# Kernel optimization log

Hardware: AMD Instinct MI355X
Metric: run time of the kernel (lower is better)

The kernel has to match this reference:

```python
import jax, jax.numpy as jnp
import numpy as np

B, D, C = 256, 128, 8000
MARGIN = 0.5
SCALE = 64.0
EPS = 1e-12  # tf.nn.l2_normalize epsilon


def _l2_normalize(x, axis):
    # Matches tf.nn.l2_normalize: x * rsqrt(max(sum(x^2), eps))
    sq = jnp.sum(x * x, axis=axis, keepdims=True)
    return x * jax.lax.rsqrt(jnp.maximum(sq, EPS))


def setup_inputs() -> dict:
    key = jax.random.key(0)
    k1, k2, k3 = jax.random.split(key, 3)
    embds = jax.random.normal(k1, (B, D), dtype=jnp.float32)
    w = jax.random.normal(k2, (D, C), dtype=jnp.float32)
    labels = jax.random.randint(k3, (B,), 0, C, dtype=jnp.int32)
    return {"embds": embds, "w": w, "labels": labels}


def reference(embds, w, labels):
    normed_embds = _l2_normalize(embds, axis=1)          # [B, D]
    normed_w = _l2_normalize(w, axis=0)                  # [D, C]
    gr_w = normed_w.T[labels]                            # gather per-label columns -> [B, D]
    # dw[b, d, c] = gr_w[b, d] - normed_w[d, c]
    dw = gr_w[:, :, None] - normed_w[None, :, :]         # [B, D, C]
    normed_dw = _l2_normalize(dw, axis=1)                # normalize over feature dim D
    win = jnp.einsum('bd,bdc->bc', normed_embds, normed_dw)
    penalties = MARGIN - jnp.minimum(MARGIN, win)        # [B, C]
    cos_t = normed_embds @ normed_w                      # [B, C]
    logits = jax.nn.softmax(SCALE * cos_t, axis=-1)
    return (logits, penalties)
```

## Files before the change

kernel.cpp:

```cpp
#include <hip/hip_runtime.h>
#include <math.h>

#define BB 256
#define DD 128
#define CC 8000
#define EPSF 1e-12f
#define SCALEF 64.0f
#define MARGINF 0.5f

__global__ __launch_bounds__(256) void prep1_kernel(
    const float* __restrict__ embds, const float* __restrict__ w,
    float* __restrict__ neT, float* __restrict__ rcol) {
  __shared__ float part[4];
  int bid = blockIdx.x;
  int tid = threadIdx.x;
  if (bid < 128) {
    int half = tid >> 7;
    int d = tid & 127;
    int r = 2 * bid + half;
    float v = embds[r * DD + d];
    float s = v * v;
    #pragma unroll
    for (int off = 32; off; off >>= 1) s += __shfl_down(s, off, 64);
    int wid = tid >> 6;
    if ((tid & 63) == 0) part[wid] = s;
    __syncthreads();
    float total = (half == 0) ? (part[0] + part[1]) : (part[2] + part[3]);
    float rn = rsqrtf(fmaxf(total, EPSF));
    neT[d * BB + r] = v * rn;
  } else {
    int c = (bid - 128) * 256 + tid;
    if (c < CC) {
      float s = 0.f;
      #pragma unroll 4
      for (int d = 0; d < DD; ++d) {
        float v = w[d * CC + c];
        s = fmaf(v, v, s);
      }
      rcol[c] = rsqrtf(fmaxf(s, EPSF));
    }
  }
}

__global__ __launch_bounds__(128) void prep2_kernel(
    const float* __restrict__ w, const int* __restrict__ labels,
    const float* __restrict__ rcol, const float* __restrict__ neT,
    float* __restrict__ gT, float* __restrict__ s1) {
  __shared__ float part[2];
  int b = blockIdx.x;
  int d = threadIdx.x;
  int lab = labels[b];
  float gv = w[d * CC + lab] * rcol[lab];
  gT[d * BB + b] = gv;
  float p = gv * neT[d * BB + b];
  #pragma unroll
  for (int off = 32; off; off >>= 1) p += __shfl_down(p, off, 64);
  if ((d & 63) == 0) part[d >> 6] = p;
  __syncthreads();
  if (d == 0) s1[b] = part[0] + part[1];
}

__global__ __launch_bounds__(256) void main_kernel(
    const float* __restrict__ w, const float* __restrict__ rcol,
    const float* __restrict__ neT, const float* __restrict__ gT,
    const float* __restrict__ s1, const int* __restrict__ labels,
    float* __restrict__ out) {
  __shared__ float neS[DD * 32];
  __shared__ float gS[DD * 32];
  int tid = threadIdx.x;
  int c0 = blockIdx.x * 256;
  int r0 = blockIdx.y * 32;

  {
    const float4* neT4 = (const float4*)neT;
    const float4* gT4 = (const float4*)gT;
    float4* neS4 = (float4*)neS;
    float4* gS4 = (float4*)gS;
    #pragma unroll
    for (int i4 = 0; i4 < 4; ++i4) {
      int idx = tid + i4 * 256;
      int d = idx >> 3;
      int r4 = idx & 7;
      int gsrc = d * (BB / 4) + (r0 >> 2) + r4;
      neS4[idx] = neT4[gsrc];
      gS4[idx] = gT4[gsrc];
    }
  }
  __syncthreads();

  int tx = tid & 63;
  int ty = tid >> 6;
  bool cok = (c0 + tx * 4) < CC;
  const float4* w4 = (const float4*)w;
  int wbase = (c0 >> 2) + tx;

  float accC[8][4];
  float accG[8][4];
  #pragma unroll
  for (int rr = 0; rr < 8; ++rr)
    #pragma unroll
    for (int j = 0; j < 4; ++j) { accC[rr][j] = 0.f; accG[rr][j] = 0.f; }

  #pragma unroll 4
  for (int d = 0; d < DD; ++d) {
    float4 wv = cok ? w4[d * (CC / 4) + wbase] : make_float4(0.f, 0.f, 0.f, 0.f);
    int base = d * 32 + ty * 8;
    float4 a0 = *(const float4*)&neS[base];
    float4 a1 = *(const float4*)&neS[base + 4];
    float4 g0 = *(const float4*)&gS[base];
    float4 g1 = *(const float4*)&gS[base + 4];
    float av[8] = {a0.x, a0.y, a0.z, a0.w, a1.x, a1.y, a1.z, a1.w};
    float gv[8] = {g0.x, g0.y, g0.z, g0.w, g1.x, g1.y, g1.z, g1.w};
    float wj[4] = {wv.x, wv.y, wv.z, wv.w};
    #pragma unroll
    for (int rr = 0; rr < 8; ++rr) {
      #pragma unroll
      for (int j = 0; j < 4; ++j) {
        accC[rr][j] = fmaf(av[rr], wj[j], accC[rr][j]);
        accG[rr][j] = fmaf(gv[rr], wj[j], accG[rr][j]);
      }
    }
  }

  if (!cok) return;
  float4 rc4 = ((const float4*)rcol)[wbase];
  float rcj[4] = {rc4.x, rc4.y, rc4.z, rc4.w};
  float* pen_base = out + (size_t)BB * CC;
  #pragma unroll
  for (int rr = 0; rr < 8; ++rr) {
    int r = r0 + ty * 8 + rr;
    float s1v = s1[r];
    int lab = labels[r];
    float cosv[4], penv[4];
    #pragma unroll
    for (int j = 0; j < 4; ++j) {
      float cs = accC[rr][j] * rcj[j];
      float gw = accG[rr][j] * rcj[j];
      float win = (s1v - cs) * rsqrtf(fmaxf(2.f - 2.f * gw, EPSF));
      int c = c0 + tx * 4 + j;
      if (c == lab) win = 0.f;
      cosv[j] = cs;
      penv[j] = MARGINF - fminf(MARGINF, win);
    }
    size_t o4 = (size_t)r * (CC / 4) + wbase;
    ((float4*)out)[o4] = make_float4(cosv[0], cosv[1], cosv[2], cosv[3]);
    ((float4*)pen_base)[o4] = make_float4(penv[0], penv[1], penv[2], penv[3]);
  }
}

__global__ __launch_bounds__(256) void softmax_kernel(float* __restrict__ out) {
  __shared__ float red[4];
  int r = blockIdx.x;
  int tid = threadIdx.x;
  float4* row = (float4*)out + (size_t)r * (CC / 4);

  float4 vals[8];
  float m = -1e30f;
  #pragma unroll
  for (int k = 0; k < 8; ++k) {
    int i = tid + k * 256;
    if (i < CC / 4) {
      float4 v = row[i];
      vals[k] = v;
      m = fmaxf(m, fmaxf(fmaxf(v.x, v.y), fmaxf(v.z, v.w)));
    }
  }
  #pragma unroll
  for (int off = 1; off < 64; off <<= 1) m = fmaxf(m, __shfl_xor(m, off, 64));
  if ((tid & 63) == 0) red[tid >> 6] = m;
  __syncthreads();
  m = fmaxf(fmaxf(red[0], red[1]), fmaxf(red[2], red[3]));
  __syncthreads();

  float s = 0.f;
  #pragma unroll
  for (int k = 0; k < 8; ++k) {
    int i = tid + k * 256;
    if (i < CC / 4) {
      float4 v = vals[k];
      float4 e;
      e.x = __expf(SCALEF * (v.x - m));
      e.y = __expf(SCALEF * (v.y - m));
      e.z = __expf(SCALEF * (v.z - m));
      e.w = __expf(SCALEF * (v.w - m));
      vals[k] = e;
      s += e.x + e.y + e.z + e.w;
    }
  }
  #pragma unroll
  for (int off = 1; off < 64; off <<= 1) s += __shfl_xor(s, off, 64);
  if ((tid & 63) == 0) red[tid >> 6] = s;
  __syncthreads();
  s = red[0] + red[1] + red[2] + red[3];
  float inv = 1.f / s;

  #pragma unroll
  for (int k = 0; k < 8; ++k) {
    int i = tid + k * 256;
    if (i < CC / 4) {
      float4 e = vals[k];
      row[i] = make_float4(e.x * inv, e.y * inv, e.z * inv, e.w * inv);
    }
  }
}

extern "C" void kernel_launch(void* const* d_in, const int* in_sizes, int n_in,
                              void* d_out, int out_size, void* d_ws, size_t ws_size,
                              hipStream_t stream) {
  const float* embds = (const float*)d_in[0];
  const float* w = (const float*)d_in[1];
  const int* labels = (const int*)d_in[2];
  float* out = (float*)d_out;
  float* ws = (float*)d_ws;

  float* neT = ws;
  float* gT = ws + 32768;
  float* rcol = ws + 65536;
  float* s1 = ws + 73536;

  prep1_kernel<<<160, 256, 0, stream>>>(embds, w, neT, rcol);
  prep2_kernel<<<256, 128, 0, stream>>>(w, labels, rcol, neT, gT, s1);
  dim3 g3(32, 8);
  main_kernel<<<g3, 256, 0, stream>>>(w, rcol, neT, gT, s1, labels, out);
  softmax_kernel<<<256, 256, 0, stream>>>(out);
}
```

Before: 107.2 us.

## Merge prep kernels, halve main-kernel row tile, widen softmax blocks

The two prep kernels become one: each label-row block now computes the gathered column's norm directly (embedding norm, label-column norm and their dot product), so the dependency on rcol and one launch disappear. The main kernel tile shrinks from 32 to 16 rows per block, doubling the grid to 512 blocks for better occupancy across CUs. The cost is that each W column tile is now streamed twice as many times. Softmax switches to 512 threads per row with fewer registers per thread.

New measurement: 95.31 us. 11.1% less time.

```diff
diff --git a/kernel.cpp b/kernel.cpp
--- a/kernel.cpp
+++ b/kernel.cpp
@@ -8,56 +8,56 @@
 #define SCALEF 64.0f
 #define MARGINF 0.5f
 
-__global__ __launch_bounds__(256) void prep1_kernel(
+__global__ __launch_bounds__(256) void prep_kernel(
     const float* __restrict__ embds, const float* __restrict__ w,
-    float* __restrict__ neT, float* __restrict__ rcol) {
-  __shared__ float part[4];
+    const int* __restrict__ labels, float* __restrict__ neT,
+    float* __restrict__ gT, float* __restrict__ rcol, float* __restrict__ s1) {
   int bid = blockIdx.x;
   int tid = threadIdx.x;
-  if (bid < 128) {
-    int half = tid >> 7;
-    int d = tid & 127;
-    int r = 2 * bid + half;
-    float v = embds[r * DD + d];
-    float s = v * v;
-    #pragma unroll
-    for (int off = 32; off; off >>= 1) s += __shfl_down(s, off, 64);
-    int wid = tid >> 6;
-    if ((tid & 63) == 0) part[wid] = s;
-    __syncthreads();
-    float total = (half == 0) ? (part[0] + part[1]) : (part[2] + part[3]);
-    float rn = rsqrtf(fmaxf(total, EPSF));
-    neT[d * BB + r] = v * rn;
-  } else {
-    int c = (bid - 128) * 256 + tid;
+  if (bid < 32) {
+    int c = bid * 256 + tid;
     if (c < CC) {
       float s = 0.f;
-      #pragma unroll 4
+      #pragma unroll 8
       for (int d = 0; d < DD; ++d) {
         float v = w[d * CC + c];
         s = fmaf(v, v, s);
       }
       rcol[c] = rsqrtf(fmaxf(s, EPSF));
     }
-  }
-}
-
-__global__ __launch_bounds__(128) void prep2_kernel(
-    const float* __restrict__ w, const int* __restrict__ labels,
-    const float* __restrict__ rcol, const float* __restrict__ neT,
-    float* __restrict__ gT, float* __restrict__ s1) {
-  __shared__ float part[2];
-  int b = blockIdx.x;
-  int d = threadIdx.x;
-  int lab = labels[b];
-  float gv = w[d * CC + lab] * rcol[lab];
-  gT[d * BB + b] = gv;
-  float p = gv * neT[d * BB + b];
-  #pragma unroll
-  for (int off = 32; off; off >>= 1) p += __shfl_down(p, off, 64);
-  if ((d & 63) == 0) part[d >> 6] = p;
-  __syncthreads();
-  if (d == 0) s1[b] = part[0] + part[1];
+  } else {
+    __shared__ float red[3][2];
+    int b = bid - 32;
+    float e = 0.f, wl = 0.f;
+    int d = tid;
+    if (tid < 128) {
+      int lab = labels[b];
+      e = embds[b * DD + d];
+      wl = w[d * CC + lab];
+      float se = e * e, sw = wl * wl, sx = e * wl;
+      #pragma unroll
+      for (int off = 32; off; off >>= 1) {
+        se += __shfl_down(se, off, 64);
+        sw += __shfl_down(sw, off, 64);
+        sx += __shfl_down(sx, off, 64);
+      }
+      if ((tid & 63) == 0) {
+        int wid = tid >> 6;
+        red[0][wid] = se; red[1][wid] = sw; red[2][wid] = sx;
+      }
+    }
+    __syncthreads();
+    if (tid < 128) {
+      float Se = red[0][0] + red[0][1];
+      float Sw = red[1][0] + red[1][1];
+      float Sx = red[2][0] + red[2][1];
+      float rn = rsqrtf(fmaxf(Se, EPSF));
+      float rl = rsqrtf(fmaxf(Sw, EPSF));
+      neT[d * BB + b] = e * rn;
+      gT[d * BB + b] = wl * rl;
+      if (tid == 0) s1[b] = Sx * rn * rl;
+    }
+  }
 }
 
 __global__ __launch_bounds__(256) void main_kernel(
@@ -65,11 +65,11 @@
     const float* __restrict__ neT, const float* __restrict__ gT,
     const float* __restrict__ s1, const int* __restrict__ labels,
     float* __restrict__ out) {
-  __shared__ float neS[DD * 32];
-  __shared__ float gS[DD * 32];
+  __shared__ float neS[DD * 16];
+  __shared__ float gS[DD * 16];
   int tid = threadIdx.x;
   int c0 = blockIdx.x * 256;
-  int r0 = blockIdx.y * 32;
+  int r0 = blockIdx.y * 16;
 
   {
     const float4* neT4 = (const float4*)neT;
@@ -77,43 +77,41 @@
     float4* neS4 = (float4*)neS;
     float4* gS4 = (float4*)gS;
     #pragma unroll
-    for (int i4 = 0; i4 < 4; ++i4) {
+    for (int i4 = 0; i4 < 2; ++i4) {
       int idx = tid + i4 * 256;
-      int d = idx >> 3;
-      int r4 = idx & 7;
-      int gsrc = d * (BB / 4) + (r0 >> 2) + r4;
-      neS4[idx] = neT4[gsrc];
-      gS4[idx] = gT4[gsrc];
+      int d = idx >> 2;
+      int r4 = idx & 3;
+      int src = d * (BB / 4) + (r0 >> 2) + r4;
+      neS4[idx] = neT4[src];
+      gS4[idx] = gT4[src];
     }
   }
   __syncthreads();
 
   int tx = tid & 63;
   int ty = tid >> 6;
-  bool cok = (c0 + tx * 4) < CC;
+  int c = c0 + tx * 4;
+  bool cok = c < CC;
   const float4* w4 = (const float4*)w;
   int wbase = (c0 >> 2) + tx;
 
-  float accC[8][4];
-  float accG[8][4];
-  #pragma unroll
-  for (int rr = 0; rr < 8; ++rr)
+  float accC[4][4];
+  float accG[4][4];
+  #pragma unroll
+  for (int rr = 0; rr < 4; ++rr)
     #pragma unroll
     for (int j = 0; j < 4; ++j) { accC[rr][j] = 0.f; accG[rr][j] = 0.f; }
 
-  #pragma unroll 4
+  #pragma unroll 8
   for (int d = 0; d < DD; ++d) {
     float4 wv = cok ? w4[d * (CC / 4) + wbase] : make_float4(0.f, 0.f, 0.f, 0.f);
-    int base = d * 32 + ty * 8;
-    float4 a0 = *(const float4*)&neS[base];
-    float4 a1 = *(const float4*)&neS[base + 4];
-    float4 g0 = *(const float4*)&gS[base];
-    float4 g1 = *(const float4*)&gS[base + 4];
-    float av[8] = {a0.x, a0.y, a0.z, a0.w, a1.x, a1.y, a1.z, a1.w};
-    float gv[8] = {g0.x, g0.y, g0.z, g0.w, g1.x, g1.y, g1.z, g1.w};
+    float4 a = *(const float4*)&neS[d * 16 + ty * 4];
+    float4 g = *(const float4*)&gS[d * 16 + ty * 4];
+    float av[4] = {a.x, a.y, a.z, a.w};
+    float gv[4] = {g.x, g.y, g.z, g.w};
     float wj[4] = {wv.x, wv.y, wv.z, wv.w};
     #pragma unroll
-    for (int rr = 0; rr < 8; ++rr) {
+    for (int rr = 0; rr < 4; ++rr) {
       #pragma unroll
       for (int j = 0; j < 4; ++j) {
         accC[rr][j] = fmaf(av[rr], wj[j], accC[rr][j]);
@@ -127,8 +125,8 @@
   float rcj[4] = {rc4.x, rc4.y, rc4.z, rc4.w};
   float* pen_base = out + (size_t)BB * CC;
   #pragma unroll
-  for (int rr = 0; rr < 8; ++rr) {
-    int r = r0 + ty * 8 + rr;
+  for (int rr = 0; rr < 4; ++rr) {
+    int r = r0 + ty * 4 + rr;
     float s1v = s1[r];
     int lab = labels[r];
     float cosv[4], penv[4];
@@ -137,8 +135,7 @@
       float cs = accC[rr][j] * rcj[j];
       float gw = accG[rr][j] * rcj[j];
       float win = (s1v - cs) * rsqrtf(fmaxf(2.f - 2.f * gw, EPSF));
-      int c = c0 + tx * 4 + j;
-      if (c == lab) win = 0.f;
+      if (c + j == lab) win = 0.f;
       cosv[j] = cs;
       penv[j] = MARGINF - fminf(MARGINF, win);
     }
@@ -148,17 +145,17 @@
   }
 }
 
-__global__ __launch_bounds__(256) void softmax_kernel(float* __restrict__ out) {
-  __shared__ float red[4];
+__global__ __launch_bounds__(512) void softmax_kernel(float* __restrict__ out) {
+  __shared__ float red[8];
   int r = blockIdx.x;
   int tid = threadIdx.x;
   float4* row = (float4*)out + (size_t)r * (CC / 4);
 
-  float4 vals[8];
+  float4 vals[4];
   float m = -1e30f;
   #pragma unroll
-  for (int k = 0; k < 8; ++k) {
-    int i = tid + k * 256;
+  for (int k = 0; k < 4; ++k) {
+    int i = tid + k * 512;
     if (i < CC / 4) {
       float4 v = row[i];
       vals[k] = v;
@@ -169,13 +166,15 @@
   for (int off = 1; off < 64; off <<= 1) m = fmaxf(m, __shfl_xor(m, off, 64));
   if ((tid & 63) == 0) red[tid >> 6] = m;
   __syncthreads();
-  m = fmaxf(fmaxf(red[0], red[1]), fmaxf(red[2], red[3]));
+  m = red[0];
+  #pragma unroll
+  for (int k = 1; k < 8; ++k) m = fmaxf(m, red[k]);
   __syncthreads();
 
   float s = 0.f;
   #pragma unroll
-  for (int k = 0; k < 8; ++k) {
-    int i = tid + k * 256;
+  for (int k = 0; k < 4; ++k) {
+    int i = tid + k * 512;
     if (i < CC / 4) {
       float4 v = vals[k];
       float4 e;
@@ -191,12 +190,14 @@
   for (int off = 1; off < 64; off <<= 1) s += __shfl_xor(s, off, 64);
   if ((tid & 63) == 0) red[tid >> 6] = s;
   __syncthreads();
-  s = red[0] + red[1] + red[2] + red[3];
+  s = red[0];
+  #pragma unroll
+  for (int k = 1; k < 8; ++k) s += red[k];
   float inv = 1.f / s;
 
   #pragma unroll
-  for (int k = 0; k < 8; ++k) {
-    int i = tid + k * 256;
+  for (int k = 0; k < 4; ++k) {
+    int i = tid + k * 512;
     if (i < CC / 4) {
       float4 e = vals[k];
       row[i] = make_float4(e.x * inv, e.y * inv, e.z * inv, e.w * inv);
@@ -218,9 +219,8 @@
   float* rcol = ws + 65536;
   float* s1 = ws + 73536;
 
-  prep1_kernel<<<160, 256, 0, stream>>>(embds, w, neT, rcol);
-  prep2_kernel<<<256, 128, 0, stream>>>(w, labels, rcol, neT, gT, s1);
-  dim3 g3(32, 8);
+  prep_kernel<<<288, 256, 0, stream>>>(embds, w, labels, neT, gT, rcol, s1);
+  dim3 g3(32, 16);
   main_kernel<<<g3, 256, 0, stream>>>(w, rcol, neT, gT, s1, labels, out);
-  softmax_kernel<<<256, 256, 0, stream>>>(out);
-}
+  softmax_kernel<<<256, 512, 0, stream>>>(out);
+}
```
